# Optimization experiments

Measured on AMD Instinct MI355X. Metric: run time of the kernel, lower is better.

The kernel has to match this reference:

```python
import jax, jax.numpy as jnp
import numpy as np

B, S, D, E = 16, 2048, 1024, 524288

def setup_inputs() -> dict:
    key = jax.random.key(0)
    k0, k1, k2, k3 = jax.random.split(key, 4)
    x = jax.random.normal(k0, (B, S, D), dtype=jnp.float32)
    mask = jnp.ones((B, S), dtype=bool)
    edges = jax.random.randint(k1, (2, E), 0, B * S, dtype=jnp.int32)
    scale = 1.0 / np.sqrt(D).astype(np.float32)
    W1 = jax.random.normal(k2, (D, D), dtype=jnp.float32) * scale  # GCNConv lin weight
    b1 = jnp.zeros((D,), dtype=jnp.float32)                        # GCNConv bias
    W2 = jax.random.normal(k3, (D, D), dtype=jnp.float32) * scale  # output Linear
    b2 = jnp.zeros((D,), dtype=jnp.float32)
    return {"x": x, "mask": mask, "edges": edges, "W1": W1, "b1": b1, "W2": W2, "b2": b2}

def reference(x, mask, edges, W1, b1, W2, b2):
    # x: [B,S,D]; mask all-True -> gather == reshape to [N,D]
    N = B * S
    nodes = x.reshape(N, D)
    src, dst = edges[0], edges[1]
    # GCN normalization (gcn_norm, add_self_loops=False): deg over dst, norm = d^-1/2[src]*d^-1/2[dst]
    deg = jax.ops.segment_sum(jnp.ones((E,), dtype=nodes.dtype), dst, num_segments=N)
    dinv = jnp.where(deg > 0, jax.lax.rsqrt(jnp.maximum(deg, 1e-12)), 0.0)
    norm = dinv[src] * dinv[dst]  # [E]
    h = nodes @ W1.T                                   # [N,D] transform
    msg = h[src] * norm[:, None]                       # [E,D] gather + scale
    agg = jax.ops.segment_sum(msg, dst, num_segments=N) + b1  # scatter-aggregate + bias
    g = jax.nn.gelu(agg, approximate=False)            # nn.GELU (exact erf)
    out = g @ W2.T + b2                                # Linear(graph_hid_dim -> input_dim)
    # residual scatter-add back into x (mask all True)
    return x + (out.reshape(B, S, D) * mask[:, :, None].astype(x.dtype))
```

## Files before the change

kernel.cpp:

```cpp
#include <hip/hip_runtime.h>
#include <stdint.h>

typedef unsigned short u16;
typedef __attribute__((ext_vector_type(8))) short s16x8;
typedef __attribute__((ext_vector_type(4))) float f32x4;

#define D_DIM 1024
#define GK 1024
#define NT 16

__device__ __forceinline__ u16 f2bf(float f) {
  union { float f; uint32_t u; } v; v.f = f;
  uint32_t u = v.u;
  return (u16)((u + 0x7FFFu + ((u >> 16) & 1u)) >> 16);
}
__device__ __forceinline__ float bf2f(u16 b) {
  union { uint32_t u; float f; } v; v.u = ((uint32_t)b) << 16;
  return v.f;
}


__device__ __forceinline__ int lds_half_off(int arr, int buf, int half) {
  return ((((arr << 1) | buf) << 1) | half) << 14;
}

__device__ __forceinline__ void stage_half(const u16* __restrict__ g, int rowBase, int kt,
                                           u16* lds, int arr, int buf, int half, int t) {
  const int hoff = lds_half_off(arr, buf, half);
#pragma unroll
  for (int j = 0; j < 2; ++j) {
    const int c = j * 512 + t;
    const int row = c >> 3;
    const int cb = ((c & 7) << 4) ^ ((row & 12) << 3);
    const u16* src = g + (size_t)(rowBase + half * 128 + row) * GK + kt * 64 + (cb >> 1);
    __builtin_amdgcn_global_load_lds((const __attribute__((address_space(1))) void*)src,
        (__attribute__((address_space(3))) void*)((char*)lds + hoff + c * 16), 16, 0, 0);
  }
}

template<int QM>
__device__ __forceinline__ void read_sub_a(const u16* lds, int buf, int half, int lane, s16x8* a) {
  const int base = lds_half_off(0, buf, half);
  const int rsel = lane & 15, cb0 = (lane >> 4) << 4;
#pragma unroll
  for (int im = 0; im < 4; ++im) {
    const int row = QM * 64 + im * 16 + rsel;
    const int swz = (row & 12) << 3;
#pragma unroll
    for (int ks = 0; ks < 2; ++ks)
      a[im * 2 + ks] = *(const s16x8*)((const char*)lds + base + row * 128 + ((ks * 64 + cb0) ^ swz));
  }
}

template<int QN>
__device__ __forceinline__ void read_sub_b(const u16* lds, int buf, int half, int rowBase, int lane, s16x8* b) {
  const int base = lds_half_off(1, buf, half);
  const int rsel = lane & 15, cb0 = (lane >> 4) << 4;
#pragma unroll
  for (int in_ = 0; in_ < 2; ++in_) {
    const int row = rowBase + (QN * 2 + in_) * 16 + rsel;
    const int swz = (row & 12) << 3;
#pragma unroll
    for (int ks = 0; ks < 2; ++ks)
      b[in_ * 2 + ks] = *(const s16x8*)((const char*)lds + base + row * 128 + ((ks * 64 + cb0) ^ swz));
  }
}

template<int QM, int QN>
__device__ __forceinline__ void do_quad(f32x4 acc[8][4], const s16x8* aS, const s16x8* bS) {
  __builtin_amdgcn_s_setprio(1);
#pragma unroll
  for (int im = 0; im < 4; ++im)
#pragma unroll
    for (int in_ = 0; in_ < 2; ++in_)
#pragma unroll
      for (int ks = 0; ks < 2; ++ks)
        acc[QM * 4 + im][QN * 2 + in_] = __builtin_amdgcn_mfma_f32_16x16x32_bf16(
            aS[im * 2 + ks], bS[in_ * 2 + ks], acc[QM * 4 + im][QN * 2 + in_], 0, 0, 0);
  __builtin_amdgcn_s_setprio(0);
}

#define BARRIER __builtin_amdgcn_s_barrier()
#define WAIT_LGKM asm volatile("s_waitcnt lgkmcnt(0)" ::: "memory")
#define WAIT_VM(n) asm volatile("s_waitcnt vmcnt(" #n ")" ::: "memory")

template<int EPI>
__global__ __launch_bounds__(512, 2) void gemm256(
    const u16* __restrict__ A, const u16* __restrict__ B, u16* __restrict__ Cb,
    const float* __restrict__ bias, const float* __restrict__ xres, float* __restrict__ Cf)
{
  __shared__ u16 lds[65536];
  const int t = threadIdx.x;
  const int lane = t & 63;
  const int w = t >> 6;
  const int wave_m = w >> 2;
  const int wave_n = w & 3;
  const int halfB = wave_n >> 1;
  const int rowBaseB = (wave_n & 1) * 64;

  const int lb = blockIdx.x;
  const int wid = ((lb & 7) << 6) | (lb >> 3);
  const int bm = wid >> 2;
  const int bn = wid & 3;
  const int rowA = bm * 256;
  const int rowB = bn * 256;

  f32x4 acc[8][4] = {};
  s16x8 aS[8], b0S[4], b1S[4];

  stage_half(A, rowA, 0, lds, 0, 0, 0, t);
  stage_half(A, rowA, 0, lds, 0, 0, 1, t);
  stage_half(B, rowB, 0, lds, 1, 0, 0, t);
  stage_half(B, rowB, 0, lds, 1, 0, 1, t);
  stage_half(B, rowB, 1, lds, 1, 1, 0, t);
  stage_half(B, rowB, 1, lds, 1, 1, 1, t);
  WAIT_VM(4);
  BARRIER;

  for (int i = 0; i < NT / 2 - 1; ++i) {
    const int t1 = 2 * i + 1;
    read_sub_a<0>(lds, 0, wave_m, lane, aS);
    read_sub_b<0>(lds, 0, halfB, rowBaseB, lane, b0S);
    stage_half(A, rowA, t1, lds, 0, 1, 0, t);
    BARRIER; WAIT_LGKM;
    do_quad<0, 0>(acc, aS, b0S);
    BARRIER;
    read_sub_b<1>(lds, 0, halfB, rowBaseB, lane, b1S);
    stage_half(A, rowA, t1, lds, 0, 1, 1, t);
    BARRIER; WAIT_LGKM;
    do_quad<0, 1>(acc, aS, b1S);
    BARRIER;
    read_sub_a<1>(lds, 0, wave_m, lane, aS);
    stage_half(B, rowB, 2 * i + 2, lds, 1, 0, 0, t);
    BARRIER; WAIT_LGKM;
    do_quad<1, 1>(acc, aS, b1S);
    BARRIER;
    stage_half(B, rowB, 2 * i + 2, lds, 1, 0, 1, t);
    WAIT_VM(4);
    BARRIER;
    do_quad<1, 0>(acc, aS, b0S);
    BARRIER;
    read_sub_a<0>(lds, 1, wave_m, lane, aS);
    read_sub_b<0>(lds, 1, halfB, rowBaseB, lane, b0S);
    stage_half(A, rowA, 2 * i + 2, lds, 0, 0, 0, t);
    BARRIER; WAIT_LGKM;
    do_quad<0, 0>(acc, aS, b0S);
    BARRIER;
    read_sub_b<1>(lds, 1, halfB, rowBaseB, lane, b1S);
    stage_half(A, rowA, 2 * i + 2, lds, 0, 0, 1, t);
    BARRIER; WAIT_LGKM;
    do_quad<0, 1>(acc, aS, b1S);
    BARRIER;
    read_sub_a<1>(lds, 1, wave_m, lane, aS);
    stage_half(B, rowB, 2 * i + 3, lds, 1, 1, 0, t);
    BARRIER; WAIT_LGKM;
    do_quad<1, 1>(acc, aS, b1S);
    BARRIER;
    stage_half(B, rowB, 2 * i + 3, lds, 1, 1, 1, t);
    WAIT_VM(4);
    BARRIER;
    do_quad<1, 0>(acc, aS, b0S);
    BARRIER;
  }

  {
    read_sub_a<0>(lds, 0, wave_m, lane, aS);
    read_sub_b<0>(lds, 0, halfB, rowBaseB, lane, b0S);
    stage_half(A, rowA, NT - 1, lds, 0, 1, 0, t);
    BARRIER; WAIT_LGKM;
    do_quad<0, 0>(acc, aS, b0S);
    BARRIER;
    read_sub_b<1>(lds, 0, halfB, rowBaseB, lane, b1S);
    stage_half(A, rowA, NT - 1, lds, 0, 1, 1, t);
    BARRIER; WAIT_LGKM;
    do_quad<0, 1>(acc, aS, b1S);
    BARRIER;
    read_sub_a<1>(lds, 0, wave_m, lane, aS);
    BARRIER; WAIT_LGKM;
    do_quad<1, 1>(acc, aS, b1S);
    BARRIER;
    WAIT_VM(0);
    BARRIER;
    do_quad<1, 0>(acc, aS, b0S);
    read_sub_a<0>(lds, 1, wave_m, lane, aS);
    read_sub_b<0>(lds, 1, halfB, rowBaseB, lane, b0S);
    WAIT_LGKM;
    do_quad<0, 0>(acc, aS, b0S);
    read_sub_b<1>(lds, 1, halfB, rowBaseB, lane, b1S);
    WAIT_LGKM;
    do_quad<0, 1>(acc, aS, b1S);
    read_sub_a<1>(lds, 1, wave_m, lane, aS);
    WAIT_LGKM;
    do_quad<1, 1>(acc, aS, b1S);
    do_quad<1, 0>(acc, aS, b0S);
  }

  const int row0 = rowA + wave_m * 128 + ((lane >> 4) << 2);
  const int col0 = rowB + wave_n * 64 + (lane & 15);
  if (EPI == 0) {
#pragma unroll
    for (int mf = 0; mf < 8; ++mf)
#pragma unroll
      for (int nf = 0; nf < 4; ++nf) {
        const int c = col0 + nf * 16;
#pragma unroll
        for (int r = 0; r < 4; ++r)
          Cb[(size_t)(row0 + mf * 16 + r) * D_DIM + c] = f2bf(acc[mf][nf][r]);
      }
  } else {
#pragma unroll
    for (int mf = 0; mf < 8; ++mf)
#pragma unroll
      for (int nf = 0; nf < 4; ++nf) {
        const int c = col0 + nf * 16;
        const float bv = bias[c];
#pragma unroll
        for (int r = 0; r < 4; ++r) {
          const size_t idx = (size_t)(row0 + mf * 16 + r) * D_DIM + c;
          Cf[idx] = acc[mf][nf][r] + bv + xres[idx];
        }
      }
  }
}

__global__ void cast_f32_bf16(const float* __restrict__ in, u16* __restrict__ out, long n) {
  long i = ((long)blockIdx.x * blockDim.x + threadIdx.x) * 4;
  if (i >= n) return;
  const float4 v = *(const float4*)(in + i);
  ushort4 o;
  o.x = f2bf(v.x); o.y = f2bf(v.y); o.z = f2bf(v.z); o.w = f2bf(v.w);
  *(ushort4*)(out + i) = o;
}

__global__ void deg_count_int(const int* __restrict__ dst, int* __restrict__ cnt, int E) {
  int i = blockIdx.x * blockDim.x + threadIdx.x;
  if (i < E) atomicAdd(&cnt[dst[i]], 1);
}

__global__ void dinv_from_cnt(const int* __restrict__ cnt, float* __restrict__ dinv, int n) {
  int i = blockIdx.x * blockDim.x + threadIdx.x;
  if (i < n) {
    int c = cnt[i];
    dinv[i] = c > 0 ? rsqrtf((float)c) : 0.f;
  }
}

__global__ __launch_bounds__(1024) void scan_offsets(const int* __restrict__ cnt,
                                                     int* __restrict__ off, int N) {
  __shared__ int part[1024];
  const int t = threadIdx.x;
  const int nper = (N + 1023) / 1024;
  const int base = t * nper;
  int s = 0;
  for (int i = 0; i < nper; ++i) {
    int idx = base + i;
    if (idx < N) s += cnt[idx];
  }
  part[t] = s;
  __syncthreads();
  for (int d = 1; d < 1024; d <<= 1) {
    int v = (t >= d) ? part[t - d] : 0;
    __syncthreads();
    part[t] += v;
    __syncthreads();
  }
  int run = (t > 0) ? part[t - 1] : 0;
  for (int i = 0; i < nper; ++i) {
    int idx = base + i;
    if (idx < N) { off[idx] = run; run += cnt[idx]; }
  }
  if (t == 1023) off[N] = run;
}

__global__ void copy_int(const int* __restrict__ a, int* __restrict__ b, int n) {
  int i = blockIdx.x * blockDim.x + threadIdx.x;
  if (i < n) b[i] = a[i];
}

__global__ void fill_csr(const int* __restrict__ src, const int* __restrict__ dst,
                         const float* __restrict__ dinv, int* __restrict__ cursor,
                         uint2* __restrict__ ebuf, int E) {
  int e = blockIdx.x * blockDim.x + threadIdx.x;
  if (e >= E) return;
  const int d = dst[e], s = src[e];
  const int pos = atomicAdd(&cursor[d], 1);
  const float nrm = dinv[s] * dinv[d];
  uint2 en; en.x = (unsigned)s; en.y = __float_as_uint(nrm);
  ebuf[pos] = en;
}

__global__ __launch_bounds__(256) void aggregate_gelu(
    const u16* __restrict__ h, const uint2* __restrict__ ebuf,
    const int* __restrict__ off, const float* __restrict__ b1,
    u16* __restrict__ g)
{
  const int d = blockIdx.x;
  const int beg = off[d], end = off[d + 1];
  __shared__ uint2 le[256];
  const int t = threadIdx.x;
  float a0 = 0.f, a1 = 0.f, a2 = 0.f, a3 = 0.f;

  for (int base = beg; base < end; base += 256) {
    const int m = min(256, end - base);
    if (t < m) le[t] = ebuf[base + t];
    __syncthreads();
    for (int i = 0; i < m; ++i) {
      const uint2 en = le[i];
      const float nrm = __uint_as_float(en.y);
      const uint2 hv = *(const uint2*)(h + (size_t)en.x * D_DIM + t * 4);
      a0 += bf2f((u16)(hv.x & 0xffffu)) * nrm;
      a1 += bf2f((u16)(hv.x >> 16)) * nrm;
      a2 += bf2f((u16)(hv.y & 0xffffu)) * nrm;
      a3 += bf2f((u16)(hv.y >> 16)) * nrm;
    }
    __syncthreads();
  }

  const int c = t * 4;
  const float t0 = a0 + b1[c], t1 = a1 + b1[c + 1], t2 = a2 + b1[c + 2], t3 = a3 + b1[c + 3];
  ushort4 o;
  o.x = f2bf(0.5f * t0 * (1.0f + erff(t0 * 0.70710678118f)));
  o.y = f2bf(0.5f * t1 * (1.0f + erff(t1 * 0.70710678118f)));
  o.z = f2bf(0.5f * t2 * (1.0f + erff(t2 * 0.70710678118f)));
  o.w = f2bf(0.5f * t3 * (1.0f + erff(t3 * 0.70710678118f)));
  *(ushort4*)(g + (size_t)d * D_DIM + c) = o;
}

extern "C" void kernel_launch(void* const* d_in, const int* in_sizes, int n_in,
                              void* d_out, int out_size, void* d_ws, size_t ws_size,
                              hipStream_t stream) {
  const float* x  = (const float*)d_in[0];
  const int* edges = (const int*)d_in[2];
  const float* W1 = (const float*)d_in[3];
  const float* b1 = (const float*)d_in[4];
  const float* W2 = (const float*)d_in[5];
  const float* b2 = (const float*)d_in[6];
  float* out = (float*)d_out;

  const int D = D_DIM;
  const long ND = (long)in_sizes[0];
  const int N = (int)(ND / D);
  const int E = in_sizes[2] / 2;
  const int* src = edges;
  const int* dst = edges + E;

  u16* xbf   = (u16*)d_ws;
  u16* hbf   = xbf + ND;
  u16* w1b   = hbf + ND;
  u16* w2b   = w1b + (size_t)D * D;
  int* cnt   = (int*)(w2b + (size_t)D * D);
  int* off   = cnt + N;
  int* cursor= off + N + 1;
  float* dnv = (float*)(cursor + N);
  uint2* ebuf= (uint2*)(dnv + N + 1);

  hipMemsetAsync(cnt, 0, (size_t)N * sizeof(int), stream);

  cast_f32_bf16<<<(int)(ND / 4 / 256), 256, 0, stream>>>(x, xbf, ND);
  cast_f32_bf16<<<(int)((long)D * D / 4 / 256), 256, 0, stream>>>(W1, w1b, (long)D * D);
  cast_f32_bf16<<<(int)((long)D * D / 4 / 256), 256, 0, stream>>>(W2, w2b, (long)D * D);

  deg_count_int<<<(E + 255) / 256, 256, 0, stream>>>(dst, cnt, E);
  dinv_from_cnt<<<(N + 255) / 256, 256, 0, stream>>>(cnt, dnv, N);
  scan_offsets<<<1, 1024, 0, stream>>>(cnt, off, N);
  copy_int<<<(N + 255) / 256, 256, 0, stream>>>(off, cursor, N);
  fill_csr<<<(E + 255) / 256, 256, 0, stream>>>(src, dst, dnv, cursor, ebuf, E);

  gemm256<0><<<(N / 256) * (D / 256), 512, 0, stream>>>(xbf, w1b, hbf, nullptr, nullptr, nullptr);

  aggregate_gelu<<<N, 256, 0, stream>>>(hbf, ebuf, off, b1, xbf);

  gemm256<1><<<(N / 256) * (D / 256), 512, 0, stream>>>(xbf, w2b, nullptr, b2, x, out);
}
```

Before: 480.8 us.

## Change LDS swizzle, fold dinv and cursor into scan, unroll aggregation

The GEMM LDS swizzle changes from XOR on row bits 2-3 to a full 3-bit XOR on row&7 across the 16-byte chunks, which is meant to spread ds_read accesses over more banks. The separate dinv and cursor-copy kernels are folded into the single-block scan kernel, saving two launches but putting more serial work into a single workgroup. The aggregation loop is unrolled by two so two gathered h rows are in flight at once.

```diff
diff --git a/kernel.cpp b/kernel.cpp
--- a/kernel.cpp
+++ b/kernel.cpp
@@ -31,7 +31,7 @@
   for (int j = 0; j < 2; ++j) {
     const int c = j * 512 + t;
     const int row = c >> 3;
-    const int cb = ((c & 7) << 4) ^ ((row & 12) << 3);
+    const int cb = (((c & 7) ^ (row & 7)) << 4);
     const u16* src = g + (size_t)(rowBase + half * 128 + row) * GK + kt * 64 + (cb >> 1);
     __builtin_amdgcn_global_load_lds((const __attribute__((address_space(1))) void*)src,
         (__attribute__((address_space(3))) void*)((char*)lds + hoff + c * 16), 16, 0, 0);
@@ -45,7 +45,7 @@
 #pragma unroll
   for (int im = 0; im < 4; ++im) {
     const int row = QM * 64 + im * 16 + rsel;
-    const int swz = (row & 12) << 3;
+    const int swz = (row & 7) << 4;
 #pragma unroll
     for (int ks = 0; ks < 2; ++ks)
       a[im * 2 + ks] = *(const s16x8*)((const char*)lds + base + row * 128 + ((ks * 64 + cb0) ^ swz));
@@ -59,7 +59,7 @@
 #pragma unroll
   for (int in_ = 0; in_ < 2; ++in_) {
     const int row = rowBase + (QN * 2 + in_) * 16 + rsel;
-    const int swz = (row & 12) << 3;
+    const int swz = (row & 7) << 4;
 #pragma unroll
     for (int ks = 0; ks < 2; ++ks)
       b[in_ * 2 + ks] = *(const s16x8*)((const char*)lds + base + row * 128 + ((ks * 64 + cb0) ^ swz));
@@ -237,16 +237,10 @@
   if (i < E) atomicAdd(&cnt[dst[i]], 1);
 }
 
-__global__ void dinv_from_cnt(const int* __restrict__ cnt, float* __restrict__ dinv, int n) {
-  int i = blockIdx.x * blockDim.x + threadIdx.x;
-  if (i < n) {
-    int c = cnt[i];
-    dinv[i] = c > 0 ? rsqrtf((float)c) : 0.f;
-  }
-}
-
 __global__ __launch_bounds__(1024) void scan_offsets(const int* __restrict__ cnt,
-                                                     int* __restrict__ off, int N) {
+                                                     int* __restrict__ off,
+                                                     int* __restrict__ cursor,
+                                                     float* __restrict__ dinv, int N) {
   __shared__ int part[1024];
   const int t = threadIdx.x;
   const int nper = (N + 1023) / 1024;
@@ -267,14 +261,15 @@
   int run = (t > 0) ? part[t - 1] : 0;
   for (int i = 0; i < nper; ++i) {
     int idx = base + i;
-    if (idx < N) { off[idx] = run; run += cnt[idx]; }
+    if (idx < N) {
+      const int c = cnt[idx];
+      off[idx] = run;
+      cursor[idx] = run;
+      dinv[idx] = c > 0 ? rsqrtf((float)c) : 0.f;
+      run += c;
+    }
   }
   if (t == 1023) off[N] = run;
-}
-
-__global__ void copy_int(const int* __restrict__ a, int* __restrict__ b, int n) {
-  int i = blockIdx.x * blockDim.x + threadIdx.x;
-  if (i < n) b[i] = a[i];
 }
 
 __global__ void fill_csr(const int* __restrict__ src, const int* __restrict__ dst,
@@ -289,6 +284,13 @@
   ebuf[pos] = en;
 }
 
+__device__ __forceinline__ void acc_row(float* a, uint2 hv, float nrm) {
+  a[0] += bf2f((u16)(hv.x & 0xffffu)) * nrm;
+  a[1] += bf2f((u16)(hv.x >> 16)) * nrm;
+  a[2] += bf2f((u16)(hv.y & 0xffffu)) * nrm;
+  a[3] += bf2f((u16)(hv.y >> 16)) * nrm;
+}
+
 __global__ __launch_bounds__(256) void aggregate_gelu(
     const u16* __restrict__ h, const uint2* __restrict__ ebuf,
     const int* __restrict__ off, const float* __restrict__ b1,
@@ -298,26 +300,30 @@
   const int beg = off[d], end = off[d + 1];
   __shared__ uint2 le[256];
   const int t = threadIdx.x;
-  float a0 = 0.f, a1 = 0.f, a2 = 0.f, a3 = 0.f;
+  float a[4] = {0.f, 0.f, 0.f, 0.f};
 
   for (int base = beg; base < end; base += 256) {
     const int m = min(256, end - base);
     if (t < m) le[t] = ebuf[base + t];
     __syncthreads();
-    for (int i = 0; i < m; ++i) {
-      const uint2 en = le[i];
-      const float nrm = __uint_as_float(en.y);
-      const uint2 hv = *(const uint2*)(h + (size_t)en.x * D_DIM + t * 4);
-      a0 += bf2f((u16)(hv.x & 0xffffu)) * nrm;
-      a1 += bf2f((u16)(hv.x >> 16)) * nrm;
-      a2 += bf2f((u16)(hv.y & 0xffffu)) * nrm;
-      a3 += bf2f((u16)(hv.y >> 16)) * nrm;
+    int i = 0;
+    for (; i + 2 <= m; i += 2) {
+      const uint2 e0 = le[i], e1 = le[i + 1];
+      const uint2 h0 = *(const uint2*)(h + (size_t)e0.x * D_DIM + t * 4);
+      const uint2 h1 = *(const uint2*)(h + (size_t)e1.x * D_DIM + t * 4);
+      acc_row(a, h0, __uint_as_float(e0.y));
+      acc_row(a, h1, __uint_as_float(e1.y));
+    }
+    if (i < m) {
+      const uint2 e0 = le[i];
+      const uint2 h0 = *(const uint2*)(h + (size_t)e0.x * D_DIM + t * 4);
+      acc_row(a, h0, __uint_as_float(e0.y));
     }
     __syncthreads();
   }
 
   const int c = t * 4;
-  const float t0 = a0 + b1[c], t1 = a1 + b1[c + 1], t2 = a2 + b1[c + 2], t3 = a3 + b1[c + 3];
+  const float t0 = a[0] + b1[c], t1 = a[1] + b1[c + 1], t2 = a[2] + b1[c + 2], t3 = a[3] + b1[c + 3];
   ushort4 o;
   o.x = f2bf(0.5f * t0 * (1.0f + erff(t0 * 0.70710678118f)));
   o.y = f2bf(0.5f * t1 * (1.0f + erff(t1 * 0.70710678118f)));
@@ -361,9 +367,7 @@
   cast_f32_bf16<<<(int)((long)D * D / 4 / 256), 256, 0, stream>>>(W2, w2b, (long)D * D);
 
   deg_count_int<<<(E + 255) / 256, 256, 0, stream>>>(dst, cnt, E);
-  dinv_from_cnt<<<(N + 255) / 256, 256, 0, stream>>>(cnt, dnv, N);
-  scan_offsets<<<1, 1024, 0, stream>>>(cnt, off, N);
-  copy_int<<<(N + 255) / 256, 256, 0, stream>>>(off, cursor, N);
+  scan_offsets<<<1, 1024, 0, stream>>>(cnt, off, cursor, dnv, N);
   fill_csr<<<(E + 255) / 256, 256, 0, stream>>>(src, dst, dnv, cursor, ebuf, E);
 
   gemm256<0><<<(N / 256) * (D / 256), 512, 0, stream>>>(xbf, w1b, hbf, nullptr, nullptr, nullptr);
```

Result: slower. 506.2 us (+5.3%).
